# Kernel optimization log

Measured on AMD Instinct MI355X. Metric: run time of the kernel, lower is better.

## Reference

```python
import jax, jax.numpy as jnp
import numpy as np

ETA_MIN = 0.02
ETA_MAX = 0.35
RHO = 0.001
NEG_INF = -1e6


def _build_transition(boundary_probs, K):
    # boundary_probs: (B, T) in [0,1]
    eta = jnp.clip(ETA_MIN + (ETA_MAX - ETA_MIN) * boundary_probs, 0.001, 0.95)  # (B,T)
    B, T = eta.shape
    dtype = eta.dtype
    idx = jnp.arange(K)
    # diagonal: row0 -> 1-eta, last row -> 1-rho, middle -> clamp(1-eta-rho, 0.01)
    stay_mid = jnp.maximum(1.0 - eta - RHO, 0.01)
    diag = jnp.broadcast_to(stay_mid[..., None], (B, T, K))
    diag = diag.at[..., 0].set(1.0 - eta)
    diag = diag.at[..., K - 1].set(1.0 - RHO)
    A = jnp.zeros((B, T, K, K), dtype=dtype)
    A = A.at[..., idx, idx].set(diag)
    # superdiagonal (rows 0..K-2): advance prob eta
    A = A.at[..., idx[:-1], idx[:-1] + 1].set(jnp.broadcast_to(eta[..., None], (B, T, K - 1)))
    # subdiagonal (rows 1..K-1): backtrack prob rho
    A = A.at[..., idx[1:], idx[1:] - 1].set(RHO)
    A = A / jnp.clip(A.sum(axis=-1, keepdims=True), 1e-8)
    return A


def setup_inputs() -> dict:
    key = jax.random.key(0)
    k1, k2 = jax.random.split(key)
    B, T, K = 32, 4096, 16
    emission_log_probs = jax.random.normal(k1, (B, T, K), dtype=jnp.float32)
    boundary_probs = jax.random.uniform(k2, (B, T), dtype=jnp.float32)
    mask = jnp.ones((B, T), dtype=jnp.float32)
    return {"emission_log_probs": emission_log_probs,
            "boundary_probs": boundary_probs,
            "mask": mask}


def reference(emission_log_probs, boundary_probs, mask):
    B, T, K = emission_log_probs.shape
    dtype = emission_log_probs.dtype
    A = _build_transition(boundary_probs, K)          # (B,T,K,K)
    log_A = jnp.log(jnp.clip(A, 1e-10))               # (B,T,K,K)

    log_alpha0 = jnp.full((B, K), NEG_INF, dtype=dtype).at[:, 0].set(0.0)

    # t = 0 (no transition)
    lj0 = log_alpha0 + emission_log_probs[:, 0]
    lZ0 = jax.nn.logsumexp(lj0, axis=-1, keepdims=True)
    la0_new = lj0 - lZ0
    m0 = mask[:, 0][:, None]
    la0 = m0 * la0_new + (1.0 - m0) * log_alpha0
    lZ0_out = mask[:, 0] * lZ0[:, 0]

    def step(log_alpha, inp):
        lA_t, em_t, m_t = inp                          # (B,K,K), (B,K), (B,)
        # logsumexp over previous-state axis i: lA_t[b,i,j] + log_alpha[b,i]
        pred = jax.nn.logsumexp(lA_t + log_alpha[:, :, None], axis=1)
        lj = pred + em_t
        lZ = jax.nn.logsumexp(lj, axis=-1, keepdims=True)
        new = lj - lZ
        m = m_t[:, None]
        log_alpha = m * new + (1.0 - m) * log_alpha
        return log_alpha, (log_alpha, m_t * lZ[:, 0])

    xs = (jnp.moveaxis(log_A, 1, 0)[1:],
          jnp.moveaxis(emission_log_probs, 1, 0)[1:],
          jnp.moveaxis(mask, 1, 0)[1:])
    _, (las, lZs) = jax.lax.scan(step, la0, xs)

    log_beliefs = jnp.moveaxis(jnp.concatenate([la0[None], las], axis=0), 0, 1)  # (B,T,K)
    log_normalizers = jnp.moveaxis(jnp.concatenate([lZ0_out[None], lZs], axis=0), 0, 1)  # (B,T)
    beliefs = jnp.exp(log_beliefs)
    return beliefs, log_beliefs, log_normalizers, A
```

## Files before the change

kernel.cpp:

```cpp
#include <hip/hip_runtime.h>


#define BB 32
#define TT 4096
#define KK 16
#define LCH 64
#define NCH 64
#define NP1 504
#define CORNER4 8192
#define NA  32736

constexpr float RHO  = 0.001f;
constexpr float LEAK = 1e-10f;

template<int CTRL>
__device__ __forceinline__ float dppf(float x) {
  return __uint_as_float((unsigned)__builtin_amdgcn_update_dpp(
      0, (int)__float_as_uint(x), CTRL, 0xF, 0xF, true));
}
__device__ __forceinline__ float sum16(float x) {
  x += dppf<0xB1>(x);
  x += dppf<0x4E>(x);
  x += dppf<0x141>(x);
  x += dppf<0x140>(x);
  return x;
}
__device__ __forceinline__ float rdfirst(float x) {
  return __uint_as_float((unsigned)__builtin_amdgcn_readfirstlane((int)__float_as_uint(x)));
}

__device__ __forceinline__ void write_A4(const float* __restrict__ bp,
                                         float* __restrict__ Aout, long tid) {
  long flat = tid * 4;
  int  bt   = (int)(flat >> 8);
  int  rem  = (int)(flat & 255);
  int  r    = rem >> 4;
  int  c0   = rem & 15;
  float p   = bp[bt];
  float eta = fminf(fmaxf(0.02f + 0.33f * p, 0.001f), 0.95f);
  float diag, s;
  if (r == 0)       { diag = 1.0f - eta; s = (1.0f - eta) + eta; }
  else if (r == 15) { diag = 1.0f - RHO; s = RHO + (1.0f - RHO); }
  else { diag = fmaxf((1.0f - eta) - RHO, 0.01f); s = (RHO + diag) + eta; }
  s = fmaxf(s, 1e-8f);
  float inv = 1.0f / s;
  float4 v;
  float* vp = &v.x;
  #pragma unroll
  for (int q = 0; q < 4; ++q) {
    int cc = c0 + q;
    float a = (cc == r) ? diag : (cc == r + 1) ? eta : (cc == r - 1) ? RHO : 0.0f;
    vp[q] = a * inv;
  }
  ((float4*)Aout)[tid] = v;
}

__global__ __launch_bounds__(256) void k1_fused(
    const float* __restrict__ em, const float* __restrict__ bp,
    const float* __restrict__ msk, float* __restrict__ Gbuf,
    float* __restrict__ Aout)
{
  const int bid = blockIdx.x;
  if (bid >= NP1) {
    long tid = (long)(bid - NP1) * 256 + threadIdx.x + CORNER4;
    write_A4(bp, Aout, tid);
    return;
  }
  int wid  = bid * 4 + (threadIdx.x >> 6);
  int lane = threadIdx.x & 63;
  int g = lane >> 4, j = lane & 15;
  int b = wid & 31;
  int c = wid >> 5;
  long t0 = (long)c * LCH + 1;
  const float* emb = em  + ((long)b * TT + t0) * KK;
  const float* bpb = bp  + (long)b * TT + t0;
  const float* mb  = msk + (long)b * TT + t0;

  float r0 = (j == 4*g + 0) ? 1.0f : 0.0f;
  float r1 = (j == 4*g + 1) ? 1.0f : 0.0f;
  float r2 = (j == 4*g + 2) ? 1.0f : 0.0f;
  float r3 = (j == 4*g + 3) ? 1.0f : 0.0f;

  float emv[4], bpv[4], mv[4];
  #pragma unroll
  for (int k = 0; k < 4; ++k) {
    emv[k] = emb[(long)k * KK + j]; bpv[k] = bpb[k]; mv[k] = mb[k];
  }
  for (int s0 = 0; s0 < LCH; s0 += 4) {
    float emn[4], bpn[4], mn[4];
    #pragma unroll
    for (int k = 0; k < 4; ++k) {
      int sn = s0 + 4 + k; if (sn > LCH - 1) sn = LCH - 1;
      emn[k] = emb[(long)sn * KK + j]; bpn[k] = bpb[sn]; mn[k] = mb[sn];
    }
    #pragma unroll
    for (int k = 0; k < 4; ++k) {
      float eta = fminf(fmaxf(fmaf(0.33f, bpv[k], 0.02f), 0.001f), 0.95f);
      float dm  = fmaxf((1.0f - eta) - RHO, 0.01f);
      float s0n = (1.0f - eta) + eta;
      float smn = (RHO + dm) + eta;
      float i0  = __builtin_amdgcn_rcpf(s0n);
      float im  = __builtin_amdgcn_rcpf(smn);
      float i_jm1 = (j == 1) ? i0 : im;
      float i_j   = (j == 0) ? i0 : ((j == 15) ? 1.0f : im);
      float i_jp1 = (j == 14) ? 1.0f : im;
      float diag  = (j == 0) ? (1.0f - eta) : ((j == 15) ? (1.0f - RHO) : dm);
      bool on  = (mv[k] != 0.0f);
      float cL = on ? eta  * i_jm1 : 0.0f;
      float cD = on ? diag * i_j   : 1.0f;
      float cR = on ? RHO  * i_jp1 : 0.0f;
      float E  = on ? __expf(emv[k]) : 1.0f;

      float pl0 = dppf<0x111>(r0), pr0 = dppf<0x101>(r0);
      float pl1 = dppf<0x111>(r1), pr1 = dppf<0x101>(r1);
      float pl2 = dppf<0x111>(r2), pr2 = dppf<0x101>(r2);
      float pl3 = dppf<0x111>(r3), pr3 = dppf<0x101>(r3);
      r0 = E * fmaf(pl0, cL, fmaf(r0, cD, pr0 * cR));
      r1 = E * fmaf(pl1, cL, fmaf(r1, cD, pr1 * cR));
      r2 = E * fmaf(pl2, cL, fmaf(r2, cD, pr2 * cR));
      r3 = E * fmaf(pl3, cL, fmaf(r3, cD, pr3 * cR));
    }
    float grand = sum16((r0 + r1) + (r2 + r3));
    grand += __shfl_xor(grand, 16);
    grand += __shfl_xor(grand, 32);
    float sc = __builtin_amdgcn_rcpf(grand);
    r0 *= sc; r1 *= sc; r2 *= sc; r3 *= sc;
    #pragma unroll
    for (int k = 0; k < 4; ++k) { emv[k] = emn[k]; bpv[k] = bpn[k]; mv[k] = mn[k]; }
  }
  float4 v; v.x = r0; v.y = r1; v.z = r2; v.w = r3;
  ((float4*)(Gbuf + ((long)(b * NCH + c) << 8)))[j * 4 + g] = v;
}

__global__ __launch_bounds__(256) void phase2_kernel(
    const float* __restrict__ em, const float* __restrict__ msk,
    const float* __restrict__ Gbuf, float* __restrict__ Pst)
{
  int b    = blockIdx.x * 4 + (threadIdx.x >> 6);
  int lane = threadIdx.x & 63;
  int g = lane >> 4, j = lane & 15;

  float em0  = em[(long)b * TT * KK + j];
  float em00 = rdfirst(em0);
  float m0   = msk[(long)b * TT];
  float la_init = (j == 0) ? 0.0f : -1000000.0f;
  float la0 = m0 * ((la_init + em0) - em00) + (1.0f - m0) * la_init;
  float P   = __expf(la0);

  const int src = 20 * g;
  float4 grow = *((const float4*)(Gbuf + ((long)(b * NCH) << 8)) + (j * 4 + g));
  for (int c = 0; c < NCH; ++c) {
    if (lane < 16) Pst[((long)(b * NCH + c) << 4) + j] = P;
    if (c == NCH - 1) break;
    float4 gnext = grow;
    if (c + 1 < NCH - 1)
      gnext = *((const float4*)(Gbuf + ((long)(b * NCH + c + 1) << 8)) + (j * 4 + g));
    float p0 = __shfl(P, src + 0), p1 = __shfl(P, src + 1);
    float p2 = __shfl(P, src + 2), p3 = __shfl(P, src + 3);
    float up = grow.x * p0;
    up = fmaf(grow.y, p1, up);
    up = fmaf(grow.z, p2, up);
    up = fmaf(grow.w, p3, up);
    up += __shfl_xor(up, 16);
    up += __shfl_xor(up, 32);
    float S = sum16(up);
    P = up * __builtin_amdgcn_rcpf(S);
    grow = gnext;
  }
}

__global__ __launch_bounds__(256) void phase3_kernel(
    const float* __restrict__ em, const float* __restrict__ bp,
    const float* __restrict__ msk, const float* __restrict__ Pst,
    float* __restrict__ out)
{
  const long BTK = (long)BB * TT * KK;
  float* beliefs = out;
  float* logb    = out + BTK;
  float* lzs     = out + 2 * BTK;

  int wid  = blockIdx.x * 4 + (threadIdx.x >> 6);
  int lane = threadIdx.x & 63;
  int j   = lane & 15;
  int row = lane >> 4;
  int b   = wid >> 4;
  int c   = ((wid & 15) << 2) + row;

  const float* emb = em  + (long)b * TT * KK;
  const float* bpb = bp  + (long)b * TT;
  const float* mb  = msk + (long)b * TT;
  float* belb = beliefs + (long)b * TT * KK;
  float* lbb  = logb    + (long)b * TT * KK;
  float* lzb  = lzs     + (long)b * TT;

  float P = Pst[((long)(b * NCH + c) << 4) + j];

  if (c == 0) {
    float em0  = emb[j];
    float em00 = rdfirst(em0);
    float m0   = mb[0];
    float la_init = (j == 0) ? 0.0f : -1000000.0f;
    float la0 = m0 * ((la_init + em0) - em00) + (1.0f - m0) * la_init;
    belb[j] = P;
    lbb[j]  = la0;
    if (j == 0) lzb[0] = m0 * em00;
  }

  const int t0 = (c << 6) + 1;
  float emv[4], bpv[4], mv[4];
  #pragma unroll
  for (int k = 0; k < 4; ++k) {
    int ts = t0 + k; if (ts > TT - 1) ts = TT - 1;
    emv[k] = emb[(long)ts * KK + j]; bpv[k] = bpb[ts]; mv[k] = mb[ts];
  }
  for (int i0 = 0; i0 < LCH; i0 += 4) {
    float emn[4], bpn[4], mn[4];
    #pragma unroll
    for (int k = 0; k < 4; ++k) {
      int ts = t0 + i0 + 4 + k; if (ts > TT - 1) ts = TT - 1;
      emn[k] = emb[(long)ts * KK + j]; bpn[k] = bpb[ts]; mn[k] = mb[ts];
    }
    #pragma unroll
    for (int k = 0; k < 4; ++k) {
      int t = t0 + i0 + k;
      float eta = fminf(fmaxf(fmaf(0.33f, bpv[k], 0.02f), 0.001f), 0.95f);
      float dm  = fmaxf((1.0f - eta) - RHO, 0.01f);
      float s0n = (1.0f - eta) + eta;
      float smn = (RHO + dm) + eta;
      float i0r = __builtin_amdgcn_rcpf(s0n);
      float im  = __builtin_amdgcn_rcpf(smn);
      float i_jm1 = (j == 1) ? i0r : im;
      float i_j   = (j == 0) ? i0r : ((j == 15) ? 1.0f : im);
      float i_jp1 = (j == 14) ? 1.0f : im;
      float diag  = (j == 0) ? (1.0f - eta) : ((j == 15) ? (1.0f - RHO) : dm);
      float cL = fmaf(eta,  i_jm1, -LEAK);
      float cD = fmaf(diag, i_j,   -LEAK);
      float cR = fmaf(RHO,  i_jp1, -LEAK);
      float E  = __expf(emv[k]);

      float pl = dppf<0x111>(P), pr = dppf<0x101>(P);
      float pred = fmaf(pl, cL, fmaf(P, cD, fmaf(pr, cR, LEAK)));
      float u = pred * E;
      float S = sum16(u);
      float Pn = u * __builtin_amdgcn_rcpf(S);
      bool on = (mv[k] != 0.0f);
      if (t < TT) {
        P = on ? Pn : P;
        belb[(long)t * KK + j] = P;
        lbb[(long)t * KK + j]  = __logf(P);
        if (j == 0) lzb[t] = on ? __logf(S) : 0.0f;
      }
    }
    #pragma unroll
    for (int k = 0; k < 4; ++k) { emv[k] = emn[k]; bpv[k] = bpn[k]; mv[k] = mn[k]; }
  }
}

__global__ __launch_bounds__(256) void a_fix_kernel(
    const float* __restrict__ bp, float* __restrict__ Aout)
{
  long tid = (long)blockIdx.x * 256 + threadIdx.x;
  write_A4(bp, Aout, tid);
}

extern "C" void kernel_launch(void* const* d_in, const int* in_sizes, int n_in,
                              void* d_out, int out_size, void* d_ws, size_t ws_size,
                              hipStream_t stream) {
  const float* em = (const float*)d_in[0];
  const float* bp = (const float*)d_in[1];
  const float* mk = (const float*)d_in[2];
  float* out = (float*)d_out;

  const long BTK = (long)BB * TT * KK;
  float* Gbuf = out;
  float* Aout = out + 2 * BTK + (long)BB * TT;
  float* Pst  = Aout;

  hipLaunchKernelGGL(k1_fused,      dim3(NP1 + NA), dim3(256), 0, stream, em, bp, mk, Gbuf, Aout);
  hipLaunchKernelGGL(phase2_kernel, dim3(8),        dim3(256), 0, stream, em, mk, Gbuf, Pst);
  hipLaunchKernelGGL(phase3_kernel, dim3(128),      dim3(256), 0, stream, em, bp, mk, Pst, out);
  hipLaunchKernelGGL(a_fix_kernel,  dim3(32),       dim3(256), 0, stream, bp, Aout);
}
```

Before: 208.6 us.

## Fuse chunk-prefix propagation into phase3 by recomputing per-wave starting states

Removes the separate serial phase2 kernel. Each phase3 wave now replays the chunk-to-chunk propagation itself, up to its own chunk, using the chunk transfer matrices, and captures its starting state. The scratch transfer matrices move from the beliefs region to the tail of the A output, which a larger fix kernel overwrites afterwards. This saves one launch and a global round trip, but adds redundant serial prefix work in phase3, up to 63 steps for the last chunks.

```diff
diff --git a/kernel.cpp b/kernel.cpp
--- a/kernel.cpp
+++ b/kernel.cpp
@@ -7,8 +7,8 @@
 #define LCH 64
 #define NCH 64
 #define NP1 504
-#define CORNER4 8192
-#define NA  32736
+#define NA  32256
+#define GOFF4 8257536L
 
 constexpr float RHO  = 0.001f;
 constexpr float LEAK = 1e-10f;
@@ -57,12 +57,12 @@
 
 __global__ __launch_bounds__(256) void k1_fused(
     const float* __restrict__ em, const float* __restrict__ bp,
-    const float* __restrict__ msk, float* __restrict__ Gbuf,
+    const float* __restrict__ msk, float* __restrict__ Gst,
     float* __restrict__ Aout)
 {
   const int bid = blockIdx.x;
   if (bid >= NP1) {
-    long tid = (long)(bid - NP1) * 256 + threadIdx.x + CORNER4;
+    long tid = (long)(bid - NP1) * 256 + threadIdx.x;
     write_A4(bp, Aout, tid);
     return;
   }
@@ -129,32 +129,50 @@
     for (int k = 0; k < 4; ++k) { emv[k] = emn[k]; bpv[k] = bpn[k]; mv[k] = mn[k]; }
   }
   float4 v; v.x = r0; v.y = r1; v.z = r2; v.w = r3;
-  ((float4*)(Gbuf + ((long)(b * NCH + c) << 8)))[j * 4 + g] = v;
-}
-
-__global__ __launch_bounds__(256) void phase2_kernel(
-    const float* __restrict__ em, const float* __restrict__ msk,
-    const float* __restrict__ Gbuf, float* __restrict__ Pst)
+  ((float4*)(Gst + ((long)(b * NCH + c) << 8)))[j * 4 + g] = v;
+}
+
+__global__ __launch_bounds__(256) void phase3_kernel(
+    const float* __restrict__ em, const float* __restrict__ bp,
+    const float* __restrict__ msk, const float* __restrict__ Gst,
+    float* __restrict__ out)
 {
-  int b    = blockIdx.x * 4 + (threadIdx.x >> 6);
+  const long BTK = (long)BB * TT * KK;
+  float* beliefs = out;
+  float* logb    = out + BTK;
+  float* lzs     = out + 2 * BTK;
+
+  int wid  = blockIdx.x * 4 + (threadIdx.x >> 6);
   int lane = threadIdx.x & 63;
-  int g = lane >> 4, j = lane & 15;
-
-  float em0  = em[(long)b * TT * KK + j];
+  int j   = lane & 15;
+  int row = lane >> 4;
+  int b   = wid >> 4;
+  int cb  = (wid & 15) << 2;
+
+  const float* emb = em  + (long)b * TT * KK;
+  const float* bpb = bp  + (long)b * TT;
+  const float* mb  = msk + (long)b * TT;
+  float* belb = beliefs + (long)b * TT * KK;
+  float* lbb  = logb    + (long)b * TT * KK;
+  float* lzb  = lzs     + (long)b * TT;
+
+  float em0  = emb[j];
   float em00 = rdfirst(em0);
-  float m0   = msk[(long)b * TT];
+  float m0   = mb[0];
   float la_init = (j == 0) ? 0.0f : -1000000.0f;
   float la0 = m0 * ((la_init + em0) - em00) + (1.0f - m0) * la_init;
   float P   = __expf(la0);
 
-  const int src = 20 * g;
-  float4 grow = *((const float4*)(Gbuf + ((long)(b * NCH) << 8)) + (j * 4 + g));
-  for (int c = 0; c < NCH; ++c) {
-    if (lane < 16) Pst[((long)(b * NCH + c) << 4) + j] = P;
-    if (c == NCH - 1) break;
-    float4 gnext = grow;
-    if (c + 1 < NCH - 1)
-      gnext = *((const float4*)(Gbuf + ((long)(b * NCH + c + 1) << 8)) + (j * 4 + g));
+  float Pcap = P;
+  const int src = 20 * row;
+  const int cstop = cb + 3;
+  float4 grow = ((const float4*)(Gst))[((long)(b * NCH) << 6) + j * 4 + row];
+  for (int c = 0; ; ++c) {
+    if (c == cb + row) Pcap = P;
+    if (c == cstop) break;
+    float4 gnx = grow;
+    if (c + 1 < cstop)
+      gnx = ((const float4*)(Gst))[((long)(b * NCH + c + 1) << 6) + j * 4 + row];
     float p0 = __shfl(P, src + 0), p1 = __shfl(P, src + 1);
     float p2 = __shfl(P, src + 2), p3 = __shfl(P, src + 3);
     float up = grow.x * p0;
@@ -165,42 +183,12 @@
     up += __shfl_xor(up, 32);
     float S = sum16(up);
     P = up * __builtin_amdgcn_rcpf(S);
-    grow = gnext;
-  }
-}
-
-__global__ __launch_bounds__(256) void phase3_kernel(
-    const float* __restrict__ em, const float* __restrict__ bp,
-    const float* __restrict__ msk, const float* __restrict__ Pst,
-    float* __restrict__ out)
-{
-  const long BTK = (long)BB * TT * KK;
-  float* beliefs = out;
-  float* logb    = out + BTK;
-  float* lzs     = out + 2 * BTK;
-
-  int wid  = blockIdx.x * 4 + (threadIdx.x >> 6);
-  int lane = threadIdx.x & 63;
-  int j   = lane & 15;
-  int row = lane >> 4;
-  int b   = wid >> 4;
-  int c   = ((wid & 15) << 2) + row;
-
-  const float* emb = em  + (long)b * TT * KK;
-  const float* bpb = bp  + (long)b * TT;
-  const float* mb  = msk + (long)b * TT;
-  float* belb = beliefs + (long)b * TT * KK;
-  float* lbb  = logb    + (long)b * TT * KK;
-  float* lzb  = lzs     + (long)b * TT;
-
-  float P = Pst[((long)(b * NCH + c) << 4) + j];
-
-  if (c == 0) {
-    float em0  = emb[j];
-    float em00 = rdfirst(em0);
-    float m0   = mb[0];
-    float la_init = (j == 0) ? 0.0f : -1000000.0f;
-    float la0 = m0 * ((la_init + em0) - em00) + (1.0f - m0) * la_init;
+    grow = gnx;
+  }
+  P = Pcap;
+  const int c = cb + row;
+
+  if (cb == 0 && lane < 16) {
     belb[j] = P;
     lbb[j]  = la0;
     if (j == 0) lzb[0] = m0 * em00;
@@ -256,10 +244,10 @@
   }
 }
 
-__global__ __launch_bounds__(256) void a_fix_kernel(
+__global__ __launch_bounds__(256) void g_fix_kernel(
     const float* __restrict__ bp, float* __restrict__ Aout)
 {
-  long tid = (long)blockIdx.x * 256 + threadIdx.x;
+  long tid = GOFF4 + (long)blockIdx.x * 256 + threadIdx.x;
   write_A4(bp, Aout, tid);
 }
 
@@ -272,12 +260,10 @@
   float* out = (float*)d_out;
 
   const long BTK = (long)BB * TT * KK;
-  float* Gbuf = out;
   float* Aout = out + 2 * BTK + (long)BB * TT;
-  float* Pst  = Aout;
-
-  hipLaunchKernelGGL(k1_fused,      dim3(NP1 + NA), dim3(256), 0, stream, em, bp, mk, Gbuf, Aout);
-  hipLaunchKernelGGL(phase2_kernel, dim3(8),        dim3(256), 0, stream, em, mk, Gbuf, Pst);
-  hipLaunchKernelGGL(phase3_kernel, dim3(128),      dim3(256), 0, stream, em, bp, mk, Pst, out);
-  hipLaunchKernelGGL(a_fix_kernel,  dim3(32),       dim3(256), 0, stream, bp, Aout);
-}
+  float* Gst  = Aout + GOFF4 * 4;
+
+  hipLaunchKernelGGL(k1_fused,      dim3(NP1 + NA), dim3(256), 0, stream, em, bp, mk, Gst, Aout);
+  hipLaunchKernelGGL(phase3_kernel, dim3(128),      dim3(256), 0, stream, em, bp, mk, Gst, out);
+  hipLaunchKernelGGL(g_fix_kernel,  dim3(512),      dim3(256), 0, stream, bp, Aout);
+}
```

Result: faster. 202.8 us (median of 2 runs) (-2.8%).
